# Kernel tuning notes

Measured on AMD Instinct MI355X. Metric: run time of the kernel, lower is better.

Reference implementation:

```python
import jax, jax.numpy as jnp
import numpy as np

N = 50000          # num_nodes
E = 800000         # num_edges (avg degree 16)
HID = 128          # hidden_dim
NH = 8             # num_heads
HD = 16            # head_dim
FFN = 512          # ffn_dim
EPS = 1e-5


def setup_inputs() -> dict:
    key = jax.random.key(0)
    ks = jax.random.split(key, 12)
    s = 0.02
    d = {}
    d["x"] = jax.random.normal(ks[0], (N, HID), jnp.float32)
    d["edge_index"] = jax.random.randint(ks[1], (2, E), 0, N, dtype=jnp.int32)
    # projection weights stored as [in, out] (math identical to torch Linear)
    d["Wq"] = jax.random.normal(ks[2], (HID, NH * HD), jnp.float32) * s
    d["bq"] = jnp.zeros((NH * HD,), jnp.float32)
    d["Wk"] = jax.random.normal(ks[3], (HID, NH * HD), jnp.float32) * s
    d["bk"] = jnp.zeros((NH * HD,), jnp.float32)
    d["Wv"] = jax.random.normal(ks[4], (HID, NH * HD), jnp.float32) * s
    d["bv"] = jnp.zeros((NH * HD,), jnp.float32)
    d["Wo"] = jax.random.normal(ks[5], (NH * HD, HID), jnp.float32) * s
    d["bo"] = jnp.zeros((HID,), jnp.float32)
    d["g1"] = jnp.ones((HID,), jnp.float32)
    d["b1"] = jnp.zeros((HID,), jnp.float32)
    d["g2"] = jnp.ones((HID,), jnp.float32)
    d["b2"] = jnp.zeros((HID,), jnp.float32)
    d["W1"] = jax.random.normal(ks[6], (HID, FFN), jnp.float32) * s
    d["bf1"] = jnp.zeros((FFN,), jnp.float32)
    d["W2"] = jax.random.normal(ks[7], (FFN, HID), jnp.float32) * s
    d["bf2"] = jnp.zeros((HID,), jnp.float32)
    return d


def _layer_norm(x, g, b):
    m = jnp.mean(x, axis=-1, keepdims=True)
    v = jnp.mean((x - m) ** 2, axis=-1, keepdims=True)
    return (x - m) * jax.lax.rsqrt(v + EPS) * g + b


def _gnn_layer(x, edge_index, Wq, bq, Wk, bk, Wv, bv, Wo, bo,
               g1, b1, g2, b2, W1, bf1, W2, bf2):
    n = x.shape[0]
    residual = x
    h = _layer_norm(x, g1, b1)

    q = (h @ Wq + bq).reshape(n, NH, HD)
    k = (h @ Wk + bk).reshape(n, NH, HD)
    v = (h @ Wv + bv).reshape(n, NH, HD)

    src, dst = edge_index[0], edge_index[1]
    # original code skips nodes with no in-neighbors (output stays zero)
    deg = jax.ops.segment_sum(jnp.ones(src.shape, x.dtype), dst, num_segments=n)
    # self-loop appended for every attended node
    loops = jnp.arange(n, dtype=src.dtype)
    s_all = jnp.concatenate([src, loops])
    d_all = jnp.concatenate([dst, loops])

    # edge-parallel scaled dot-product scores: [E+N, NH]
    e = jnp.sum(q[d_all] * k[s_all], axis=-1) / np.sqrt(HD).astype(np.float32)
    m = jax.lax.stop_gradient(jax.ops.segment_max(e, d_all, num_segments=n))
    p = jnp.exp(e - m[d_all])
    z = jax.ops.segment_sum(p, d_all, num_segments=n)
    alpha = p / z[d_all]                                   # segment softmax
    agg = jax.ops.segment_sum(alpha[:, :, None] * v[s_all], d_all,
                              num_segments=n)              # [n, NH, HD]
    agg = jnp.where(deg[:, None, None] > 0, agg, jnp.zeros_like(agg))

    att = agg.reshape(n, NH * HD) @ Wo + bo
    x = residual + att                                     # dropout=0 (eval)

    residual = x
    h = _layer_norm(x, g2, b2)
    ffn = jax.nn.gelu(h @ W1 + bf1, approximate=False) @ W2 + bf2
    return residual + ffn


def reference(x, edge_index, Wq, bq, Wk, bk, Wv, bv, Wo, bo,
              g1, b1, g2, b2, W1, bf1, W2, bf2):
    return _gnn_layer(x, edge_index, Wq, bq, Wk, bk, Wv, bv, Wo, bo,
                      g1, b1, g2, b2, W1, bf1, W2, bf2)
```

## Files before the change

kernel.cpp:

```cpp
#include <hip/hip_runtime.h>
#include <hip/hip_bf16.h>

typedef __hip_bfloat16 bf16;
typedef __attribute__((ext_vector_type(8))) short s16x8;
typedef __attribute__((ext_vector_type(4))) float f32x4;

__device__ __forceinline__ float2 bfpair(unsigned u) {
    float2 r;
    r.x = __uint_as_float(u << 16);
    r.y = __uint_as_float(u & 0xffff0000u);
    return r;
}

__device__ __forceinline__ unsigned short f2bf_bits(float f) {
    unsigned u = __float_as_uint(f);
    return (unsigned short)((u + 0x7fffu + ((u >> 16) & 1u)) >> 16);
}

typedef const __attribute__((address_space(1))) unsigned GU;
typedef __attribute__((address_space(3))) unsigned LU;
__device__ __forceinline__ void gload_lds16(const void* g, void* l) {
    __builtin_amdgcn_global_load_lds((GU*)g, (LU*)l, 16, 0, 0);
}

__global__ __launch_bounds__(256) void zero_k(float* __restrict__ p, long long n) {
    long long i = (long long)blockIdx.x * 256 + threadIdx.x;
    long long st = (long long)gridDim.x * 256;
    for (; i < n; i += st) p[i] = 0.f;
}

__global__ __launch_bounds__(256) void canon_ei_k(const unsigned* __restrict__ src,
                                                  int* __restrict__ dst, int twoE) {
    __shared__ int s_nz;
    if (threadIdx.x == 0) s_nz = 0;
    __syncthreads();
    if (src[2 * threadIdx.x + 1] != 0u) atomicAdd(&s_nz, 1);
    __syncthreads();
    bool is64 = (s_nz == 0);
    long long i = (long long)blockIdx.x * 256 + threadIdx.x;
    long long st = (long long)gridDim.x * 256;
    if (is64) { for (; i < twoE; i += st) dst[i] = (int)src[2 * i]; }
    else      { for (; i < twoE; i += st) dst[i] = (int)src[i]; }
}

__global__ __launch_bounds__(256) void count_deg_k(const int* __restrict__ ei,
                                                   int* __restrict__ deg, int E) {
    int e = blockIdx.x * 256 + threadIdx.x;
    if (e < E) atomicAdd(&deg[ei[E + e]], 1);
}

#define SCAN_BLK 1024
__global__ __launch_bounds__(256) void scan1_k(const int* __restrict__ deg,
                                               int* __restrict__ off,
                                               int* __restrict__ bsum, int n) {
    __shared__ int s[256];
    int base = blockIdx.x * SCAN_BLK;
    int t = threadIdx.x;
    int v[4]; int sum = 0;
    #pragma unroll
    for (int j = 0; j < 4; j++) {
        int idx = base + t * 4 + j;
        v[j] = (idx < n) ? deg[idx] : 0;
        sum += v[j];
    }
    s[t] = sum; __syncthreads();
    for (int o = 1; o < 256; o <<= 1) {
        int add = (t >= o) ? s[t - o] : 0;
        __syncthreads();
        s[t] += add;
        __syncthreads();
    }
    int run = (t > 0) ? s[t - 1] : 0;
    if (t == 255) bsum[blockIdx.x] = s[255];
    #pragma unroll
    for (int j = 0; j < 4; j++) {
        int idx = base + t * 4 + j;
        if (idx < n) off[idx] = run;
        run += v[j];
    }
}

__global__ __launch_bounds__(64) void scan2_k(int* __restrict__ bsum, int nb) {
    int t = threadIdx.x;
    int own = (t < nb) ? bsum[t] : 0;
    int v = own;
    #pragma unroll
    for (int o = 1; o < 64; o <<= 1) {
        int u = __shfl_up(v, o);
        if (t >= o) v += u;
    }
    if (t < nb) bsum[t] = v - own;
}

__global__ __launch_bounds__(256) void scan3_k(int* __restrict__ off,
                                               int* __restrict__ cursor,
                                               const int* __restrict__ bsum, int n) {
    int i = blockIdx.x * 256 + threadIdx.x;
    if (i < n) {
        int o = off[i] + bsum[i / SCAN_BLK];
        off[i] = o;
        cursor[i] = o;
    }
}

__global__ __launch_bounds__(256) void scatter_k(const int* __restrict__ ei,
                                                 int* __restrict__ cursor,
                                                 int* __restrict__ csr, int E) {
    int e = blockIdx.x * 256 + threadIdx.x;
    if (e >= E) return;
    int s = ei[e], d = ei[E + e];
    int pos = atomicAdd(&cursor[d], 1);
    csr[pos] = s;
}

__global__ __launch_bounds__(256) void ln_bf16_k(const float* __restrict__ x,
                                                 const float* __restrict__ g,
                                                 const float* __restrict__ b,
                                                 bf16* __restrict__ out, int M) {
    int row = blockIdx.x * 4 + (threadIdx.x >> 6);
    if (row >= M) return;
    int lane = threadIdx.x & 63;
    float2 f = ((const float2*)x)[(size_t)row * 64 + lane];
    float s = f.x + f.y;
    #pragma unroll
    for (int off = 32; off > 0; off >>= 1) s += __shfl_xor(s, off);
    float mean = s * (1.0f / 128.0f);
    float d0 = f.x - mean, d1 = f.y - mean;
    float vs = d0 * d0 + d1 * d1;
    #pragma unroll
    for (int off = 32; off > 0; off >>= 1) vs += __shfl_xor(vs, off);
    float rstd = rsqrtf(vs * (1.0f / 128.0f) + 1e-5f);
    float2 gg = ((const float2*)g)[lane];
    float2 bb = ((const float2*)b)[lane];
    float o0 = d0 * rstd * gg.x + bb.x;
    float o1 = d1 * rstd * gg.y + bb.y;
    unsigned pk = ((unsigned)f2bf_bits(o1) << 16) | (unsigned)f2bf_bits(o0);
    ((unsigned*)out)[(size_t)row * 64 + lane] = pk;
}

__global__ __launch_bounds__(256) void prepw_k(const float* __restrict__ Wq,
                                               const float* __restrict__ Wk,
                                               const float* __restrict__ Wv,
                                               const float* __restrict__ Wo,
                                               const float* __restrict__ W1,
                                               const float* __restrict__ W2,
                                               const float* __restrict__ bq,
                                               const float* __restrict__ bk,
                                               const float* __restrict__ bv,
                                               unsigned short* __restrict__ qkvH,
                                               unsigned short* __restrict__ qkvL,
                                               unsigned short* __restrict__ woH,
                                               unsigned short* __restrict__ woL,
                                               unsigned short* __restrict__ w1H,
                                               unsigned short* __restrict__ w1L,
                                               unsigned short* __restrict__ w2H,
                                               unsigned short* __restrict__ w2L,
                                               float* __restrict__ bqkv) {
    int idx = blockIdx.x * 256 + threadIdx.x;
    if (idx >= 196608) {
        int i = idx - 196608;
        if (i < 384) bqkv[i] = (i < 128) ? bq[i] : (i < 256) ? bk[i - 128] : bv[i - 256];
        return;
    }
    float w; unsigned short *H, *L; int oi;
    if (idx < 49152) {
        int n = idx >> 7, kx = idx & 127;
        const float* W = (n < 128) ? Wq : (n < 256) ? Wk : Wv;
        w = W[kx * 128 + (n & 127)];
        H = qkvH; L = qkvL; oi = idx;
    } else if (idx < 65536) {
        int li = idx - 49152; int n = li >> 7, kx = li & 127;
        w = Wo[kx * 128 + n]; H = woH; L = woL; oi = li;
    } else if (idx < 131072) {
        int li = idx - 65536; int n = li >> 7, kx = li & 127;
        w = W1[(size_t)kx * 512 + n]; H = w1H; L = w1L; oi = li;
    } else {
        int li = idx - 131072; int n = li >> 9, kx = li & 511;
        w = W2[(size_t)kx * 128 + n]; H = w2H; L = w2L; oi = li;
    }
    unsigned short hbits = f2bf_bits(w);
    float hf = __uint_as_float((unsigned)hbits << 16);
    H[oi] = hbits;
    L[oi] = f2bf_bits(w - hf);
}

template <int EPI, bool OUTBF, int K, int BM>
__global__ __launch_bounds__(256) void mgemm_k(const bf16* __restrict__ A,
                                               const bf16* __restrict__ Bh,
                                               const bf16* __restrict__ Bl,
                                               const float* __restrict__ bias,
                                               const float* __restrict__ res,
                                               void* __restrict__ outp,
                                               long long sub_off, int M,
                                               int ldo, int sub_shift) {
    constexpr int MF = BM / 32;
    constexpr int NK = K / 64;
    constexpr int ABYTES = BM * 128;
    __shared__ __align__(16) char smem[ABYTES + 32768];

    const int lane = threadIdx.x & 63;
    const int wid  = threadIdx.x >> 6;
    const int wr = wid >> 1, wc = wid & 1;
    const int lrow = lane & 15, lk = lane >> 4;
    const int mw0 = wr * (BM / 2);
    const int n0 = blockIdx.x * 128 + wc * 64;
    const int nblk0 = blockIdx.x * 128;
    const int rsub = lane >> 3;
    const int swz16 = (((lane & 7) ^ rsub) - (lane & 7)) * 16;

    f32x4 acc[MF][4];
    #pragma unroll
    for (int mf = 0; mf < MF; mf++)
        #pragma unroll
        for (int nf = 0; nf < 4; nf++) {
            f32x4 z = {0.f, 0.f, 0.f, 0.f};
            acc[mf][nf] = z;
        }

    const char* Ab  = (const char*)A  + (size_t)blockIdx.y * BM * (K * 2);
    const char* Bhb = (const char*)Bh + (size_t)nblk0 * (K * 2);
    const char* Blb = (const char*)Bl + (size_t)nblk0 * (K * 2);
    const int laneByte = (lane & 7) * 16;

    #pragma unroll
    for (int kt = 0; kt < NK; kt++) {
        const int kb = kt * 128;
        #pragma unroll
        for (int it = 0; it < BM / 32; it++) {
            int rg = wid * (BM / 4) + it * 8;
            gload_lds16(Ab + (size_t)(rg + rsub) * (K * 2) + kb + laneByte + swz16,
                        &smem[rg * 128]);
        }
        #pragma unroll
        for (int it = 0; it < 4; it++) {
            int rg = wid * 32 + it * 8;
            gload_lds16(Bhb + (size_t)(rg + rsub) * (K * 2) + kb + laneByte + swz16,
                        &smem[ABYTES + rg * 128]);
            gload_lds16(Blb + (size_t)(rg + rsub) * (K * 2) + kb + laneByte + swz16,
                        &smem[ABYTES + 16384 + rg * 128]);
        }
        __syncthreads();
        #pragma unroll
        for (int ki = 0; ki < 2; ki++) {
            s16x8 a[MF], bh[4], bl[4];
            #pragma unroll
            for (int mf = 0; mf < MF; mf++) {
                int ra = mw0 + mf * 16 + lrow;
                a[mf] = *(const s16x8*)&smem[ra * 128 + (((lk + 4 * ki) ^ (ra & 7)) * 16)];
            }
            #pragma unroll
            for (int nf = 0; nf < 4; nf++) {
                int rb = wc * 64 + nf * 16 + lrow;
                int co = ((lk + 4 * ki) ^ (rb & 7)) * 16;
                bh[nf] = *(const s16x8*)&smem[ABYTES + rb * 128 + co];
                bl[nf] = *(const s16x8*)&smem[ABYTES + 16384 + rb * 128 + co];
            }
            #pragma unroll
            for (int mf = 0; mf < MF; mf++)
                #pragma unroll
                for (int nf = 0; nf < 4; nf++)
                    acc[mf][nf] = __builtin_amdgcn_mfma_f32_16x16x32_bf16(a[mf], bh[nf], acc[mf][nf], 0, 0, 0);
            #pragma unroll
            for (int mf = 0; mf < MF; mf++)
                #pragma unroll
                for (int nf = 0; nf < 4; nf++)
                    acc[mf][nf] = __builtin_amdgcn_mfma_f32_16x16x32_bf16(a[mf], bl[nf], acc[mf][nf], 0, 0, 0);
        }
        __syncthreads();
    }

    const int nmask = (1 << sub_shift) - 1;
    #pragma unroll
    for (int mf = 0; mf < MF; mf++) {
        #pragma unroll
        for (int nf = 0; nf < 4; nf++) {
            int n = n0 + nf * 16 + lrow;
            float bsv = bias[n];
            #pragma unroll
            for (int r = 0; r < 4; r++) {
                int m = blockIdx.y * BM + mw0 + mf * 16 + lk * 4 + r;
                if (m >= M) continue;
                float val = acc[mf][nf][r] + bsv;
                if (EPI == 1) val = 0.5f * val * (1.0f + erff(val * 0.70710678118f));
                if (EPI == 2) val += res[(size_t)m * ldo + n];
                long long oidx = (long long)m * ldo + (n & nmask) + (long long)(n >> sub_shift) * sub_off;
                if (OUTBF) ((unsigned short*)outp)[oidx] = f2bf_bits(val);
                else       ((float*)outp)[oidx] = val;
            }
        }
    }
}

__global__ __launch_bounds__(256) void node_agg_k(const bf16* __restrict__ q,
                                                  const bf16* __restrict__ k,
                                                  const bf16* __restrict__ v,
                                                  const int* __restrict__ off,
                                                  const int* __restrict__ deg,
                                                  const int* __restrict__ csr,
                                                  bf16* __restrict__ agg, int NN) {
    int node = blockIdx.x * 4 + (threadIdx.x >> 6);
    if (node >= NN) return;
    int lane = threadIdx.x & 63;
    float2 qf = bfpair(((const unsigned*)(q + (size_t)node * 128))[lane]);
    int start = off[node];
    int cnt = deg[node];
    float acc0 = 0.f, acc1 = 0.f, zsum = 0.f;
    if (cnt < 64) {
        int T = cnt + 1;
        int s_vec = (lane < cnt) ? csr[start + lane] : node;
        for (int e0 = 0; e0 < T; e0 += 8) {
            unsigned ku[8], vu[8];
            #pragma unroll
            for (int j = 0; j < 8; j++) {
                if (e0 + j < T) {
                    int s = __shfl(s_vec, e0 + j);
                    ku[j] = ((const unsigned*)(k + (size_t)s * 128))[lane];
                    vu[j] = ((const unsigned*)(v + (size_t)s * 128))[lane];
                }
            }
            #pragma unroll
            for (int j = 0; j < 8; j++) {
                if (e0 + j < T) {
                    float2 kf = bfpair(ku[j]);
                    float dot = qf.x * kf.x + qf.y * kf.y;
                    dot += __shfl_xor(dot, 1);
                    dot += __shfl_xor(dot, 2);
                    dot += __shfl_xor(dot, 4);
                    float p = __expf(dot * 0.25f);
                    zsum += p;
                    float2 vf = bfpair(vu[j]);
                    acc0 += p * vf.x;
                    acc1 += p * vf.y;
                }
            }
        }
    } else {
        for (int e = 0; e <= cnt; e++) {
            int s = (e < cnt) ? csr[start + e] : node;
            float2 kf = bfpair(((const unsigned*)(k + (size_t)s * 128))[lane]);
            float dot = qf.x * kf.x + qf.y * kf.y;
            dot += __shfl_xor(dot, 1);
            dot += __shfl_xor(dot, 2);
            dot += __shfl_xor(dot, 4);
            float p = __expf(dot * 0.25f);
            zsum += p;
            float2 vf = bfpair(((const unsigned*)(v + (size_t)s * 128))[lane]);
            acc0 += p * vf.x;
            acc1 += p * vf.y;
        }
    }
    float2 o;
    if (cnt == 0) { o.x = 0.f; o.y = 0.f; }
    else { float inv = 1.0f / zsum; o.x = acc0 * inv; o.y = acc1 * inv; }
    unsigned pk = ((unsigned)f2bf_bits(o.y) << 16) | (unsigned)f2bf_bits(o.x);
    ((unsigned*)agg)[(size_t)node * 64 + lane] = pk;
}

extern "C" void kernel_launch(void* const* d_in, const int* in_sizes, int n_in,
                              void* d_out, int out_size, void* d_ws, size_t ws_size,
                              hipStream_t stream) {
    const float* x  = (const float*)d_in[0];
    const void*  eiRaw = d_in[1];
    const float* Wq = (const float*)d_in[2];
    const float* bq = (const float*)d_in[3];
    const float* Wk = (const float*)d_in[4];
    const float* bk = (const float*)d_in[5];
    const float* Wv = (const float*)d_in[6];
    const float* bv = (const float*)d_in[7];
    const float* Wo = (const float*)d_in[8];
    const float* bo = (const float*)d_in[9];
    const float* g1 = (const float*)d_in[10];
    const float* b1 = (const float*)d_in[11];
    const float* g2 = (const float*)d_in[12];
    const float* b2 = (const float*)d_in[13];
    const float* W1 = (const float*)d_in[14];
    const float* bf1 = (const float*)d_in[15];
    const float* W2 = (const float*)d_in[16];
    const float* bf2 = (const float*)d_in[17];
    float* out = (float*)d_out;

    const int N = in_sizes[0] / 128;
    const int E = in_sizes[1] / 2;
    const int gy = (N + 127) / 128;
    const int gy64 = (N + 63) / 64;
    const int Mp = gy * 128;

    char* w = (char*)d_ws;
    size_t off_b = 0;
    auto alloc = [&](size_t bytes) -> void* {
        void* ptr = w + off_b;
        off_b = (off_b + bytes + 255) & ~(size_t)255;
        return ptr;
    };
    int*   deg    = (int*)alloc((size_t)N * 4);
    int*   offA   = (int*)alloc((size_t)N * 4);
    int*   cursor = (int*)alloc((size_t)N * 4);
    int*   bsum   = (int*)alloc(64 * 4);
    int*   ei32   = (int*)alloc((size_t)E * 2 * 4);
    int*   csr    = (int*)alloc((size_t)E * 4);
    bf16*  hb     = (bf16*)alloc((size_t)Mp * 128 * 2);
    bf16*  qkvb   = (bf16*)alloc((size_t)N * 3 * 128 * 2);
    bf16*  aggb   = (bf16*)alloc((size_t)Mp * 128 * 2);
    bf16*  t      = (bf16*)alloc((size_t)Mp * 512 * 2);
    unsigned short* qkvH = (unsigned short*)alloc(49152 * 2);
    unsigned short* qkvL = (unsigned short*)alloc(49152 * 2);
    unsigned short* woH  = (unsigned short*)alloc(16384 * 2);
    unsigned short* woL  = (unsigned short*)alloc(16384 * 2);
    unsigned short* w1H  = (unsigned short*)alloc(65536 * 2);
    unsigned short* w1L  = (unsigned short*)alloc(65536 * 2);
    unsigned short* w2H  = (unsigned short*)alloc(65536 * 2);
    unsigned short* w2L  = (unsigned short*)alloc(65536 * 2);
    float* bqkv = (float*)alloc(384 * 4);
    (void)ws_size; (void)n_in; (void)out_size;

    int nb = (N + SCAN_BLK - 1) / SCAN_BLK;

    zero_k<<<64, 256, 0, stream>>>((float*)deg, N);
    canon_ei_k<<<2048, 256, 0, stream>>>((const unsigned*)eiRaw, ei32, E * 2);
    count_deg_k<<<(E + 255) / 256, 256, 0, stream>>>(ei32, deg, E);
    scan1_k<<<nb, 256, 0, stream>>>(deg, offA, bsum, N);
    scan2_k<<<1, 64, 0, stream>>>(bsum, nb);
    scan3_k<<<(N + 255) / 256, 256, 0, stream>>>(offA, cursor, bsum, N);
    scatter_k<<<(E + 255) / 256, 256, 0, stream>>>(ei32, cursor, csr, E);

    prepw_k<<<770, 256, 0, stream>>>(Wq, Wk, Wv, Wo, W1, W2, bq, bk, bv,
                                     qkvH, qkvL, woH, woL, w1H, w1L, w2H, w2L, bqkv);

    int lnBlocks = (N + 3) / 4;
    bf16* qb = qkvb;
    bf16* kb = qkvb + (size_t)N * 128;
    bf16* vb = qkvb + (size_t)N * 256;

    ln_bf16_k<<<lnBlocks, 256, 0, stream>>>(x, g1, b1, hb, N);
    mgemm_k<0, true, 128, 128><<<dim3(3, gy), 256, 0, stream>>>(
        hb, (const bf16*)qkvH, (const bf16*)qkvL, bqkv, nullptr, qkvb,
        (long long)N * 128, N, 128, 7);
    node_agg_k<<<(N + 3) / 4, 256, 0, stream>>>(qb, kb, vb, offA, deg, csr, aggb, N);
    mgemm_k<2, false, 128, 64><<<dim3(1, gy64), 256, 0, stream>>>(
        aggb, (const bf16*)woH, (const bf16*)woL, bo, x, out, 0, N, 128, 15);
    ln_bf16_k<<<lnBlocks, 256, 0, stream>>>(out, g2, b2, hb, N);
    mgemm_k<1, true, 128, 128><<<dim3(4, gy), 256, 0, stream>>>(
        hb, (const bf16*)w1H, (const bf16*)w1L, bf1, nullptr, t, 0, N, 512, 15);
    mgemm_k<2, false, 512, 64><<<dim3(1, gy64), 256, 0, stream>>>(
        t, (const bf16*)w2H, (const bf16*)w2L, bf2, out, out, 0, N, 128, 15);
}
```

Measured before the change: 408.0 us.

## Merge setup kernels, fuse LayerNorm into Wo GEMM, double-buffer GEMM K-loop

Several changes land together. The weight prep, degree zeroing and edge-index canonicalisation run as one setup kernel, and the tiny scan2 kernel is folded into scan3. The Wo-projection GEMM now applies the residual and the second LayerNorm in its epilogue and writes the bf16 normalized activations directly, so one ln_bf16 pass is dropped. The GEMM main loop switches from single-buffered 64-wide K tiles to double-buffered 32-wide K tiles so loads can overlap MFMA work. The aims are fewer launches and less memory traffic, at the cost of more LDS use and more sync steps, plus a one-pass variance formula (E[x²]−mean²) in the fused LayerNorm.

```diff
diff --git a/kernel.cpp b/kernel.cpp
--- a/kernel.cpp
+++ b/kernel.cpp
@@ -23,24 +23,74 @@
     __builtin_amdgcn_global_load_lds((GU*)g, (LU*)l, 16, 0, 0);
 }
 
-__global__ __launch_bounds__(256) void zero_k(float* __restrict__ p, long long n) {
-    long long i = (long long)blockIdx.x * 256 + threadIdx.x;
-    long long st = (long long)gridDim.x * 256;
-    for (; i < n; i += st) p[i] = 0.f;
-}
-
-__global__ __launch_bounds__(256) void canon_ei_k(const unsigned* __restrict__ src,
-                                                  int* __restrict__ dst, int twoE) {
+__global__ __launch_bounds__(256) void setup_k(const float* __restrict__ Wq,
+                                               const float* __restrict__ Wk,
+                                               const float* __restrict__ Wv,
+                                               const float* __restrict__ Wo,
+                                               const float* __restrict__ W1,
+                                               const float* __restrict__ W2,
+                                               const float* __restrict__ bq,
+                                               const float* __restrict__ bk,
+                                               const float* __restrict__ bv,
+                                               unsigned short* __restrict__ qkvH,
+                                               unsigned short* __restrict__ qkvL,
+                                               unsigned short* __restrict__ woH,
+                                               unsigned short* __restrict__ woL,
+                                               unsigned short* __restrict__ w1H,
+                                               unsigned short* __restrict__ w1L,
+                                               unsigned short* __restrict__ w2H,
+                                               unsigned short* __restrict__ w2L,
+                                               float* __restrict__ bqkv,
+                                               int* __restrict__ deg,
+                                               const unsigned* __restrict__ eisrc,
+                                               int* __restrict__ ei32,
+                                               int N, int twoE, int nzero) {
+    int b = blockIdx.x;
+    int tid = threadIdx.x;
+    if (b < 770) {
+        int idx = b * 256 + tid;
+        if (idx >= 196608) {
+            int i = idx - 196608;
+            if (i < 384) bqkv[i] = (i < 128) ? bq[i] : (i < 256) ? bk[i - 128] : bv[i - 256];
+            return;
+        }
+        float w; unsigned short *H, *L; int oi;
+        if (idx < 49152) {
+            int n = idx >> 7, kx = idx & 127;
+            const float* W = (n < 128) ? Wq : (n < 256) ? Wk : Wv;
+            w = W[kx * 128 + (n & 127)];
+            H = qkvH; L = qkvL; oi = idx;
+        } else if (idx < 65536) {
+            int li = idx - 49152; int n = li >> 7, kx = li & 127;
+            w = Wo[kx * 128 + n]; H = woH; L = woL; oi = li;
+        } else if (idx < 131072) {
+            int li = idx - 65536; int n = li >> 7, kx = li & 127;
+            w = W1[(size_t)kx * 512 + n]; H = w1H; L = w1L; oi = li;
+        } else {
+            int li = idx - 131072; int n = li >> 9, kx = li & 511;
+            w = W2[(size_t)kx * 128 + n]; H = w2H; L = w2L; oi = li;
+        }
+        unsigned short hbits = f2bf_bits(w);
+        float hf = __uint_as_float((unsigned)hbits << 16);
+        H[oi] = hbits;
+        L[oi] = f2bf_bits(w - hf);
+        return;
+    }
+    if (b < 770 + nzero) {
+        int i = (b - 770) * 256 + tid;
+        if (i < N) deg[i] = 0;
+        return;
+    }
     __shared__ int s_nz;
-    if (threadIdx.x == 0) s_nz = 0;
+    if (tid == 0) s_nz = 0;
     __syncthreads();
-    if (src[2 * threadIdx.x + 1] != 0u) atomicAdd(&s_nz, 1);
+    if (eisrc[2 * tid + 1] != 0u) atomicAdd(&s_nz, 1);
     __syncthreads();
     bool is64 = (s_nz == 0);
-    long long i = (long long)blockIdx.x * 256 + threadIdx.x;
-    long long st = (long long)gridDim.x * 256;
-    if (is64) { for (; i < twoE; i += st) dst[i] = (int)src[2 * i]; }
-    else      { for (; i < twoE; i += st) dst[i] = (int)src[i]; }
+    long long i = (long long)(b - 770 - nzero) * 256 + tid;
+    long long st = (long long)2000 * 256;
+    if (is64) { for (; i < twoE; i += st) ei32[i] = (int)eisrc[2 * i]; }
+    else      { for (; i < twoE; i += st) ei32[i] = (int)eisrc[i]; }
 }
 
 __global__ __launch_bounds__(256) void count_deg_k(const int* __restrict__ ei,
@@ -80,24 +130,26 @@
     }
 }
 
-__global__ __launch_bounds__(64) void scan2_k(int* __restrict__ bsum, int nb) {
-    int t = threadIdx.x;
-    int own = (t < nb) ? bsum[t] : 0;
-    int v = own;
-    #pragma unroll
-    for (int o = 1; o < 64; o <<= 1) {
-        int u = __shfl_up(v, o);
-        if (t >= o) v += u;
-    }
-    if (t < nb) bsum[t] = v - own;
-}
-
 __global__ __launch_bounds__(256) void scan3_k(int* __restrict__ off,
                                                int* __restrict__ cursor,
-                                               const int* __restrict__ bsum, int n) {
-    int i = blockIdx.x * 256 + threadIdx.x;
+                                               const int* __restrict__ bsum,
+                                               int n, int nb) {
+    __shared__ int sb[64];
+    int t = threadIdx.x;
+    if (t < 64) {
+        int own = (t < nb) ? bsum[t] : 0;
+        int v = own;
+        #pragma unroll
+        for (int o = 1; o < 64; o <<= 1) {
+            int u = __shfl_up(v, o);
+            if ((t & 63) >= o) v += u;
+        }
+        sb[t] = v - own;
+    }
+    __syncthreads();
+    int i = blockIdx.x * 256 + t;
     if (i < n) {
-        int o = off[i] + bsum[i / SCAN_BLK];
+        int o = off[i] + sb[i / SCAN_BLK];
         off[i] = o;
         cursor[i] = o;
     }
@@ -138,75 +190,36 @@
     ((unsigned*)out)[(size_t)row * 64 + lane] = pk;
 }
 
-__global__ __launch_bounds__(256) void prepw_k(const float* __restrict__ Wq,
-                                               const float* __restrict__ Wk,
-                                               const float* __restrict__ Wv,
-                                               const float* __restrict__ Wo,
-                                               const float* __restrict__ W1,
-                                               const float* __restrict__ W2,
-                                               const float* __restrict__ bq,
-                                               const float* __restrict__ bk,
-                                               const float* __restrict__ bv,
-                                               unsigned short* __restrict__ qkvH,
-                                               unsigned short* __restrict__ qkvL,
-                                               unsigned short* __restrict__ woH,
-                                               unsigned short* __restrict__ woL,
-                                               unsigned short* __restrict__ w1H,
-                                               unsigned short* __restrict__ w1L,
-                                               unsigned short* __restrict__ w2H,
-                                               unsigned short* __restrict__ w2L,
-                                               float* __restrict__ bqkv) {
-    int idx = blockIdx.x * 256 + threadIdx.x;
-    if (idx >= 196608) {
-        int i = idx - 196608;
-        if (i < 384) bqkv[i] = (i < 128) ? bq[i] : (i < 256) ? bk[i - 128] : bv[i - 256];
-        return;
-    }
-    float w; unsigned short *H, *L; int oi;
-    if (idx < 49152) {
-        int n = idx >> 7, kx = idx & 127;
-        const float* W = (n < 128) ? Wq : (n < 256) ? Wk : Wv;
-        w = W[kx * 128 + (n & 127)];
-        H = qkvH; L = qkvL; oi = idx;
-    } else if (idx < 65536) {
-        int li = idx - 49152; int n = li >> 7, kx = li & 127;
-        w = Wo[kx * 128 + n]; H = woH; L = woL; oi = li;
-    } else if (idx < 131072) {
-        int li = idx - 65536; int n = li >> 7, kx = li & 127;
-        w = W1[(size_t)kx * 512 + n]; H = w1H; L = w1L; oi = li;
-    } else {
-        int li = idx - 131072; int n = li >> 9, kx = li & 511;
-        w = W2[(size_t)kx * 128 + n]; H = w2H; L = w2L; oi = li;
-    }
-    unsigned short hbits = f2bf_bits(w);
-    float hf = __uint_as_float((unsigned)hbits << 16);
-    H[oi] = hbits;
-    L[oi] = f2bf_bits(w - hf);
-}
-
-template <int EPI, bool OUTBF, int K, int BM>
+template <int EPI, bool OUTBF, int K, int BM, bool LNF>
 __global__ __launch_bounds__(256) void mgemm_k(const bf16* __restrict__ A,
                                                const bf16* __restrict__ Bh,
                                                const bf16* __restrict__ Bl,
                                                const float* __restrict__ bias,
                                                const float* __restrict__ res,
                                                void* __restrict__ outp,
+                                               const float* __restrict__ lg,
+                                               const float* __restrict__ lb,
+                                               bf16* __restrict__ hbout,
                                                long long sub_off, int M,
                                                int ldo, int sub_shift) {
     constexpr int MF = BM / 32;
-    constexpr int NK = K / 64;
-    constexpr int ABYTES = BM * 128;
-    __shared__ __align__(16) char smem[ABYTES + 32768];
+    constexpr int NK = K / 32;
+    constexpr int STEP = BM * 64 + 2 * 8192;
+    __shared__ __align__(16) char smem[2 * STEP];
 
     const int lane = threadIdx.x & 63;
     const int wid  = threadIdx.x >> 6;
     const int wr = wid >> 1, wc = wid & 1;
     const int lrow = lane & 15, lk = lane >> 4;
+    const int m0 = blockIdx.y * BM;
     const int mw0 = wr * (BM / 2);
     const int n0 = blockIdx.x * 128 + wc * 64;
-    const int nblk0 = blockIdx.x * 128;
-    const int rsub = lane >> 3;
-    const int swz16 = (((lane & 7) ^ rsub) - (lane & 7)) * 16;
+    const int srow = lane >> 2;
+    const int schunk = (lane & 3) ^ (srow & 3);
+
+    const char* Ab  = (const char*)A  + (size_t)m0 * (K * 2);
+    const char* Bhb = (const char*)Bh + (size_t)(blockIdx.x * 128) * (K * 2);
+    const char* Blb = (const char*)Bl + (size_t)(blockIdx.x * 128) * (K * 2);
 
     f32x4 acc[MF][4];
     #pragma unroll
@@ -217,75 +230,140 @@
             acc[mf][nf] = z;
         }
 
-    const char* Ab  = (const char*)A  + (size_t)blockIdx.y * BM * (K * 2);
-    const char* Bhb = (const char*)Bh + (size_t)nblk0 * (K * 2);
-    const char* Blb = (const char*)Bl + (size_t)nblk0 * (K * 2);
-    const int laneByte = (lane & 7) * 16;
-
-    #pragma unroll
+    auto stage = [&](int kt, int bufb) {
+        const int kb = kt * 64;
+        char* sb = &smem[bufb];
+        #pragma unroll
+        for (int it = 0; it < BM / 64; it++) {
+            int rg = wid * (BM / 4) + it * 16;
+            gload_lds16(Ab + (size_t)(rg + srow) * (K * 2) + kb + schunk * 16,
+                        sb + rg * 64);
+        }
+        #pragma unroll
+        for (int it = 0; it < 2; it++) {
+            int rg = wid * 32 + it * 16;
+            gload_lds16(Bhb + (size_t)(rg + srow) * (K * 2) + kb + schunk * 16,
+                        sb + BM * 64 + rg * 64);
+            gload_lds16(Blb + (size_t)(rg + srow) * (K * 2) + kb + schunk * 16,
+                        sb + BM * 64 + 8192 + rg * 64);
+        }
+    };
+
+    auto compute = [&](int bufb) {
+        const char* sb = &smem[bufb];
+        s16x8 a[MF], bh[4], bl[4];
+        #pragma unroll
+        for (int mf = 0; mf < MF; mf++) {
+            int ra = mw0 + mf * 16 + lrow;
+            a[mf] = *(const s16x8*)(sb + ra * 64 + ((lk ^ (ra & 3)) * 16));
+        }
+        #pragma unroll
+        for (int nf = 0; nf < 4; nf++) {
+            int rb = wc * 64 + nf * 16 + lrow;
+            int co = (lk ^ (rb & 3)) * 16;
+            bh[nf] = *(const s16x8*)(sb + BM * 64 + rb * 64 + co);
+            bl[nf] = *(const s16x8*)(sb + BM * 64 + 8192 + rb * 64 + co);
+        }
+        #pragma unroll
+        for (int mf = 0; mf < MF; mf++)
+            #pragma unroll
+            for (int nf = 0; nf < 4; nf++)
+                acc[mf][nf] = __builtin_amdgcn_mfma_f32_16x16x32_bf16(a[mf], bh[nf], acc[mf][nf], 0, 0, 0);
+        #pragma unroll
+        for (int mf = 0; mf < MF; mf++)
+            #pragma unroll
+            for (int nf = 0; nf < 4; nf++)
+                acc[mf][nf] = __builtin_amdgcn_mfma_f32_16x16x32_bf16(a[mf], bl[nf], acc[mf][nf], 0, 0, 0);
+    };
+
+    stage(0, 0);
     for (int kt = 0; kt < NK; kt++) {
-        const int kb = kt * 128;
-        #pragma unroll
-        for (int it = 0; it < BM / 32; it++) {
-            int rg = wid * (BM / 4) + it * 8;
-            gload_lds16(Ab + (size_t)(rg + rsub) * (K * 2) + kb + laneByte + swz16,
-                        &smem[rg * 128]);
-        }
-        #pragma unroll
-        for (int it = 0; it < 4; it++) {
-            int rg = wid * 32 + it * 8;
-            gload_lds16(Bhb + (size_t)(rg + rsub) * (K * 2) + kb + laneByte + swz16,
-                        &smem[ABYTES + rg * 128]);
-            gload_lds16(Blb + (size_t)(rg + rsub) * (K * 2) + kb + laneByte + swz16,
-                        &smem[ABYTES + 16384 + rg * 128]);
-        }
         __syncthreads();
-        #pragma unroll
-        for (int ki = 0; ki < 2; ki++) {
-            s16x8 a[MF], bh[4], bl[4];
-            #pragma unroll
-            for (int mf = 0; mf < MF; mf++) {
-                int ra = mw0 + mf * 16 + lrow;
-                a[mf] = *(const s16x8*)&smem[ra * 128 + (((lk + 4 * ki) ^ (ra & 7)) * 16)];
+        if (kt + 1 < NK) stage(kt + 1, ((kt + 1) & 1) * STEP);
+        compute((kt & 1) * STEP);
+    }
+
+    if (!LNF) {
+        const int nmask = (1 << sub_shift) - 1;
+        #pragma unroll
+        for (int mf = 0; mf < MF; mf++) {
+            #pragma unroll
+            for (int nf = 0; nf < 4; nf++) {
+                int n = n0 + nf * 16 + lrow;
+                float bsv = bias[n];
+                #pragma unroll
+                for (int r = 0; r < 4; r++) {
+                    int m = m0 + mw0 + mf * 16 + lk * 4 + r;
+                    if (m >= M) continue;
+                    float val = acc[mf][nf][r] + bsv;
+                    if (EPI == 1) val = 0.5f * val * (1.0f + erff(val * 0.70710678118f));
+                    if (EPI == 2) val += res[(size_t)m * ldo + n];
+                    long long oidx = (long long)m * ldo + (n & nmask) + (long long)(n >> sub_shift) * sub_off;
+                    if (OUTBF) ((unsigned short*)outp)[oidx] = f2bf_bits(val);
+                    else       ((float*)outp)[oidx] = val;
+                }
             }
-            #pragma unroll
-            for (int nf = 0; nf < 4; nf++) {
-                int rb = wc * 64 + nf * 16 + lrow;
-                int co = ((lk + 4 * ki) ^ (rb & 7)) * 16;
-                bh[nf] = *(const s16x8*)&smem[ABYTES + rb * 128 + co];
-                bl[nf] = *(const s16x8*)&smem[ABYTES + 16384 + rb * 128 + co];
+        }
+    } else {
+        float vals[MF][4][4];
+        float s1[MF][4], s2[MF][4];
+        #pragma unroll
+        for (int mf = 0; mf < MF; mf++)
+            #pragma unroll
+            for (int r = 0; r < 4; r++) { s1[mf][r] = 0.f; s2[mf][r] = 0.f; }
+        #pragma unroll
+        for (int mf = 0; mf < MF; mf++) {
+            #pragma unroll
+            for (int r = 0; r < 4; r++) {
+                int m = m0 + mw0 + mf * 16 + lk * 4 + r;
+                #pragma unroll
+                for (int nf = 0; nf < 4; nf++) {
+                    int n = n0 + nf * 16 + lrow;
+                    float val = acc[mf][nf][r] + bias[n];
+                    val += (m < M) ? res[(size_t)m * 128 + n] : 0.f;
+                    vals[mf][nf][r] = val;
+                    s1[mf][r] += val;
+                    s2[mf][r] += val * val;
+                }
+                #pragma unroll
+                for (int o = 1; o < 16; o <<= 1) {
+                    s1[mf][r] += __shfl_xor(s1[mf][r], o);
+                    s2[mf][r] += __shfl_xor(s2[mf][r], o);
+                }
             }
+        }
+        float2* lns = (float2*)smem;
+        __syncthreads();
+        if (lrow == 0) {
             #pragma unroll
             for (int mf = 0; mf < MF; mf++)
                 #pragma unroll
-                for (int nf = 0; nf < 4; nf++)
-                    acc[mf][nf] = __builtin_amdgcn_mfma_f32_16x16x32_bf16(a[mf], bh[nf], acc[mf][nf], 0, 0, 0);
-            #pragma unroll
-            for (int mf = 0; mf < MF; mf++)
+                for (int r = 0; r < 4; r++) {
+                    int rl = mw0 + mf * 16 + lk * 4 + r;
+                    float2 p; p.x = s1[mf][r]; p.y = s2[mf][r];
+                    lns[rl * 2 + wc] = p;
+                }
+        }
+        __syncthreads();
+        #pragma unroll
+        for (int mf = 0; mf < MF; mf++) {
+            #pragma unroll
+            for (int r = 0; r < 4; r++) {
+                int rl = mw0 + mf * 16 + lk * 4 + r;
+                int m = m0 + rl;
+                float2 pa = lns[rl * 2 + 0], pb = lns[rl * 2 + 1];
+                float mean = (pa.x + pb.x) * (1.0f / 128.0f);
+                float var  = (pa.y + pb.y) * (1.0f / 128.0f) - mean * mean;
+                float rstd = rsqrtf(var + 1e-5f);
+                if (m >= M) continue;
                 #pragma unroll
-                for (int nf = 0; nf < 4; nf++)
-                    acc[mf][nf] = __builtin_amdgcn_mfma_f32_16x16x32_bf16(a[mf], bl[nf], acc[mf][nf], 0, 0, 0);
-        }
-        __syncthreads();
-    }
-
-    const int nmask = (1 << sub_shift) - 1;
-    #pragma unroll
-    for (int mf = 0; mf < MF; mf++) {
-        #pragma unroll
-        for (int nf = 0; nf < 4; nf++) {
-            int n = n0 + nf * 16 + lrow;
-            float bsv = bias[n];
-            #pragma unroll
-            for (int r = 0; r < 4; r++) {
-                int m = blockIdx.y * BM + mw0 + mf * 16 + lk * 4 + r;
-                if (m >= M) continue;
-                float val = acc[mf][nf][r] + bsv;
-                if (EPI == 1) val = 0.5f * val * (1.0f + erff(val * 0.70710678118f));
-                if (EPI == 2) val += res[(size_t)m * ldo + n];
-                long long oidx = (long long)m * ldo + (n & nmask) + (long long)(n >> sub_shift) * sub_off;
-                if (OUTBF) ((unsigned short*)outp)[oidx] = f2bf_bits(val);
-                else       ((float*)outp)[oidx] = val;
+                for (int nf = 0; nf < 4; nf++) {
+                    int n = n0 + nf * 16 + lrow;
+                    float val = vals[mf][nf][r];
+                    ((float*)outp)[(size_t)m * 128 + n] = val;
+                    float o = (val - mean) * rstd * lg[n] + lb[n];
+                    ((unsigned short*)hbout)[(size_t)m * 128 + n] = f2bf_bits(o);
+                }
             }
         }
     }
@@ -414,33 +492,33 @@
     (void)ws_size; (void)n_in; (void)out_size;
 
     int nb = (N + SCAN_BLK - 1) / SCAN_BLK;
-
-    zero_k<<<64, 256, 0, stream>>>((float*)deg, N);
-    canon_ei_k<<<2048, 256, 0, stream>>>((const unsigned*)eiRaw, ei32, E * 2);
+    int nzero = (N + 255) / 256;
+
+    setup_k<<<770 + nzero + 2000, 256, 0, stream>>>(
+        Wq, Wk, Wv, Wo, W1, W2, bq, bk, bv,
+        qkvH, qkvL, woH, woL, w1H, w1L, w2H, w2L, bqkv,
+        deg, (const unsigned*)eiRaw, ei32, N, E * 2, nzero);
     count_deg_k<<<(E + 255) / 256, 256, 0, stream>>>(ei32, deg, E);
     scan1_k<<<nb, 256, 0, stream>>>(deg, offA, bsum, N);
-    scan2_k<<<1, 64, 0, stream>>>(bsum, nb);
-    scan3_k<<<(N + 255) / 256, 256, 0, stream>>>(offA, cursor, bsum, N);
+    scan3_k<<<(N + 255) / 256, 256, 0, stream>>>(offA, cursor, bsum, N, nb);
     scatter_k<<<(E + 255) / 256, 256, 0, stream>>>(ei32, cursor, csr, E);
 
-    prepw_k<<<770, 256, 0, stream>>>(Wq, Wk, Wv, Wo, W1, W2, bq, bk, bv,
-                                     qkvH, qkvL, woH, woL, w1H, w1L, w2H, w2L, bqkv);
-
-    int lnBlocks = (N + 3) / 4;
     bf16* qb = qkvb;
     bf16* kb = qkvb + (size_t)N * 128;
     bf16* vb = qkvb + (size_t)N * 256;
 
-    ln_bf16_k<<<lnBlocks, 256, 0, stream>>>(x, g1, b1, hb, N);
-    mgemm_k<0, true, 128, 128><<<dim3(3, gy), 256, 0, stream>>>(
+    ln_bf16_k<<<(N + 3) / 4, 256, 0, stream>>>(x, g1, b1, hb, N);
+    mgemm_k<0, true, 128, 128, false><<<dim3(3, gy), 256, 0, stream>>>(
         hb, (const bf16*)qkvH, (const bf16*)qkvL, bqkv, nullptr, qkvb,
-        (long long)N * 128, N, 128, 7);
+        nullptr, nullptr, nullptr, (long long)N * 128, N, 128, 7);
     node_agg_k<<<(N + 3) / 4, 256, 0, stream>>>(qb, kb, vb, offA, deg, csr, aggb, N);
-    mgemm_k<2, false, 128, 64><<<dim3(1, gy64), 256, 0, stream>>>(
-        aggb, (const bf16*)woH, (const bf16*)woL, bo, x, out, 0, N, 128, 15);
-    ln_bf16_k<<<lnBlocks, 256, 0, stream>>>(out, g2, b2, hb, N);
-    mgemm_k<1, true, 128, 128><<<dim3(4, gy), 256, 0, stream>>>(
-        hb, (const bf16*)w1H, (const bf16*)w1L, bf1, nullptr, t, 0, N, 512, 15);
-    mgemm_k<2, false, 512, 64><<<dim3(1, gy64), 256, 0, stream>>>(
-        t, (const bf16*)w2H, (const bf16*)w2L, bf2, out, out, 0, N, 128, 15);
-}
+    mgemm_k<2, false, 128, 64, true><<<dim3(1, gy64), 256, 0, stream>>>(
+        aggb, (const bf16*)woH, (const bf16*)woL, bo, x, out,
+        g2, b2, hb, 0, N, 128, 15);
+    mgemm_k<1, true, 128, 128, false><<<dim3(4, gy), 256, 0, stream>>>(
+        hb, (const bf16*)w1H, (const bf16*)w1L, bf1, nullptr, t,
+        nullptr, nullptr, nullptr, 0, N, 512, 15);
+    mgemm_k<2, false, 512, 64, false><<<dim3(1, gy64), 256, 0, stream>>>(
+        t, (const bf16*)w2H, (const bf16*)w2L, bf2, out, out,
+        nullptr, nullptr, nullptr, 0, N, 128, 15);
+}
```

After: 394.8 us. 3.2% less time.
